# Kernel optimization log

Measured on AMD Instinct MI355X. Metric: run time of the kernel, lower is better.

The kernel has to match this reference:

```python
import jax, jax.numpy as jnp
import numpy as np

B, SQ, SK, D = 8, 2048, 2048, 128


def setup_inputs() -> dict:
    key = jax.random.key(0)
    kq, kk, kv = jax.random.split(key, 3)
    Q = jax.random.normal(kq, (B, SQ, D), dtype=jnp.float32)
    K = jax.random.normal(kk, (B, SK, D), dtype=jnp.float32)
    V = jax.random.normal(kv, (B, SK, D), dtype=jnp.float32)
    return {"Q": Q, "K": K, "V": V}


def reference(Q, K, V):
    d_k = K.shape[2]  # NOTE: module divides by d_k, not sqrt(d_k)
    # scores: [B, Sq, Sk]
    scores = jnp.einsum('bqd,bkd->bqk', Q, K) / d_k
    # unconventional softmax over the batch dim (dim=0), as in the source
    attn = jax.nn.softmax(scores, axis=0)
    # output: [B, Sq, D]
    return jnp.einsum('bqk,bkd->bqd', attn, V)
```

## Files before the change

kernel.cpp:

```cpp
#include <hip/hip_runtime.h>
#include <hip/hip_bf16.h>

#define B_   8
#define SQ_  2048
#define SK_  2048
#define D_   128

typedef __attribute__((ext_vector_type(8))) _Float16 f16x8;
typedef __attribute__((ext_vector_type(4))) _Float16 f16x4;
typedef __attribute__((ext_vector_type(4))) float    f32x4;

#define QK_BSTRIDE (128 * 4 * 64 * 8)
#define VF_BSTRIDE (64 * 8 * 64 * 8)

__device__ __forceinline__ void dma16(const void* g, void* l) {
    __builtin_amdgcn_global_load_lds(
        (const __attribute__((address_space(1))) unsigned int*)g,
        (__attribute__((address_space(3))) unsigned int*)l, 16, 0, 0);
}

__device__ __forceinline__ float fast_exp2(float x) {
#if __has_builtin(__builtin_amdgcn_exp2f)
    return __builtin_amdgcn_exp2f(x);
#else
    return __expf(x * 0.6931471805599453f);
#endif
}

__global__ __launch_bounds__(256)
void prep(const float* __restrict__ Q, const float* __restrict__ K,
          const float* __restrict__ V,
          _Float16* __restrict__ Qf, _Float16* __restrict__ Kf,
          _Float16* __restrict__ Vf) {
    __shared__ _Float16 T[64][136];
    const int bid = blockIdx.x;
    const int t   = threadIdx.x;
    if (bid < 512) {
        const int tens = bid >> 8;
        const float* src = tens ? K : Q;
        _Float16*    dst = tens ? Kf : Qf;
        const float  sc  = tens ? 0.0625f : 0.18033688f;
        const int b  = (bid >> 5) & 7;
        const int rb = bid & 31;
        const int row = t >> 2, c0 = (t & 3) * 32;
        const float* srow = src + ((size_t)b * 2048 + rb * 64 + row) * 128 + c0;
#pragma unroll
        for (int u = 0; u < 32; u += 4) {
            f32x4 v = *(const f32x4*)(srow + u);
            f16x4 h;
            h[0] = (_Float16)(v[0] * sc); h[1] = (_Float16)(v[1] * sc);
            h[2] = (_Float16)(v[2] * sc); h[3] = (_Float16)(v[3] * sc);
            *(f16x4*)&T[row][c0 + u] = h;
        }
        __syncthreads();
#pragma unroll
        for (int u = 0; u < 4; ++u) {
            int c  = u * 256 + t;
            int l  = c & 63;
            int ks = (c >> 6) & 3;
            int qt = c >> 8;
            int hi = l >> 4, ql = l & 15;
            f16x8 r = *(const f16x8*)&T[qt * 16 + ql][ks * 32 + hi * 8];
            *(f16x8*)(dst + ((((size_t)b * 128 + rb * 4 + qt) * 4 + ks) * 64 + l) * 8) = r;
        }
    } else {
        const int vb = bid - 512;
        const int b  = vb >> 5;
        const int kb = vb & 31;
        const int row = t >> 2, c0 = (t & 3) * 32;
        const float* src = V + ((size_t)b * SK_ + kb * 64 + row) * D_ + c0;
#pragma unroll
        for (int u = 0; u < 8; ++u) {
            f32x4 v = *(const f32x4*)(src + u * 4);
            f16x4 h;
            h[0] = (_Float16)v[0]; h[1] = (_Float16)v[1];
            h[2] = (_Float16)v[2]; h[3] = (_Float16)v[3];
            *(f16x4*)&T[row][c0 + u * 4] = h;
        }
        __syncthreads();
#pragma unroll
        for (int u = 0; u < 4; ++u) {
            int s   = u * 256 + t;
            int l   = s & 63;
            int dt  = (s >> 6) & 7;
            int ktl = s >> 9;
            int hi  = l >> 4, ql = l & 15;
            f16x8 r;
#pragma unroll
            for (int j = 0; j < 8; ++j) r[j] = T[ktl * 32 + hi * 8 + j][dt * 16 + ql];
            *(f16x8*)(Vf + (((size_t)b * 64 + kb * 2 + ktl) * 8 + dt) * 512 + (size_t)l * 8) = r;
        }
    }
}

__global__ __launch_bounds__(512, 4)
void zred(const _Float16* __restrict__ Qf, const _Float16* __restrict__ Kf,
          _Float16* __restrict__ Pf, int nqt, int qoff16) {
    __shared__ __attribute__((aligned(16))) _Float16 E[8][64][64];
    const int bid   = blockIdx.x;
    const int qtile = bid >> 5;
    const int ktile = bid & 31;
    const int b  = threadIdx.x >> 6;
    const int l  = threadIdx.x & 63;
    const int hi = l >> 4, ql = l & 15;

    const _Float16* Qb = Qf + (size_t)b * QK_BSTRIDE;
    const _Float16* Kb = Kf + (size_t)b * QK_BSTRIDE;

    f32x4 s[4][4] = {};
    __builtin_amdgcn_s_setprio(1);
#pragma unroll
    for (int ks = 0; ks < 4; ++ks) {
        f16x8 kf[4];
#pragma unroll
        for (int kk = 0; kk < 4; ++kk)
            kf[kk] = *(const f16x8*)(Kb + ((((size_t)ktile * 4 + kk) * 4 + ks) * 64 + l) * 8);
#pragma unroll
        for (int qq = 0; qq < 4; ++qq) {
            f16x8 qv = *(const f16x8*)(Qb + ((((size_t)(qoff16 + qtile * 4 + qq)) * 4 + ks) * 64 + l) * 8);
#pragma unroll
            for (int kk = 0; kk < 4; ++kk)
                s[kk][qq] = __builtin_amdgcn_mfma_f32_16x16x32_f16(kf[kk], qv, s[kk][qq], 0, 0, 0);
        }
    }
    __builtin_amdgcn_s_setprio(0);

    f16x4* E4 = (f16x4*)&E[0][0][0];
#pragma unroll
    for (int kk = 0; kk < 4; ++kk)
#pragma unroll
        for (int qq = 0; qq < 4; ++qq) {
            f16x4 e;
#pragma unroll
            for (int r = 0; r < 4; ++r)
                e[r] = (_Float16)fast_exp2(s[kk][qq][r]);
            int q = qq * 16 + ql;
            int k = kk * 16 + hi * 4;
            int g16 = ((b * 64 + q) << 3) + ((k >> 3) ^ (q & 7));
            E4[g16 * 2 + ((k >> 2) & 1)] = e;
        }
    __syncthreads();

    const int t    = threadIdx.x;
    const int ktl  = t >> 8;
    const int qq2  = (t >> 6) & 3;
    const int l2   = t & 63;
    const int hi2  = l2 >> 4, ql2 = l2 & 15;
    const int q_loc  = qq2 * 16 + ql2;
    const int k0_loc = ktl * 32 + hi2 * 8;
    const f16x8* E8  = (const f16x8*)&E[0][0][0];
    const int eidx   = (q_loc << 3) + ((k0_loc >> 3) ^ (q_loc & 7));

    f16x8 z = E8[eidx];
#pragma unroll
    for (int bb = 1; bb < 8; ++bb) z = z + E8[bb * 512 + eidx];
    float inv[8];
#pragma unroll
    for (int j = 0; j < 8; ++j) inv[j] = __builtin_amdgcn_rcpf((float)z[j]);

    const size_t pbase = (((size_t)(qtile * 4 + qq2)) * 64 + (ktile * 2 + ktl)) * 512 + (size_t)l2 * 8;
#pragma unroll
    for (int bb = 0; bb < 8; ++bb) {
        f16x8 e = E8[bb * 512 + eidx];
        f16x8 p;
#pragma unroll
        for (int j = 0; j < 8; ++j) p[j] = (_Float16)((float)e[j] * inv[j]);
        *(f16x8*)(Pf + (size_t)bb * nqt * 32768 + pbase) = p;
    }
}

__global__ __launch_bounds__(512)
void av(const _Float16* __restrict__ Pf, const _Float16* __restrict__ Vf,
        float* __restrict__ out, int nqt, int qoff) {
    __shared__ __attribute__((aligned(16))) _Float16 lds[4 * 12288];

    const int bid = blockIdx.x;
    const int b   = bid & 7;
    const int mt  = bid >> 3;
    const int w   = threadIdx.x >> 6;
    const int l   = threadIdx.x & 63;
    const int wq  = w >> 2;
    const int wd  = w & 3;
    const int hi  = l >> 4, ql = l & 15;

    const _Float16* Pb = Pf + (size_t)b * nqt * 32768;
    const _Float16* Vb = Vf + (size_t)b * VF_BSTRIDE;

#define STAGE(bufi, kt2) do {                                                  \
    _Float16* dst0 = (_Float16*)lds + (size_t)(bufi) * 12288;                  \
    _Pragma("unroll")                                                          \
    for (int u = 0; u < 3; ++u) {                                              \
        int c = w * 3 + u;                                                     \
        const _Float16* srcp;                                                  \
        if (c < 8)                                                             \
            srcp = Pb + (((size_t)(mt * 4 + (c >> 1))) * 64 + ((kt2) * 2 + (c & 1))) * 512 + (size_t)l * 8; \
        else {                                                                 \
            int cv = c - 8;                                                    \
            srcp = Vb + (((size_t)((kt2) * 2 + (cv >> 3))) * 8 + (cv & 7)) * 512 + (size_t)l * 8; \
        }                                                                      \
        dma16(srcp, dst0 + c * 512);                                           \
    }                                                                          \
} while (0)

#define MFMA_PHASE(bufi) do {                                                  \
    const _Float16* Bf = (const _Float16*)lds + (size_t)(bufi) * 12288;        \
    _Pragma("unroll")                                                          \
    for (int ktl = 0; ktl < 2; ++ktl) {                                        \
        f16x8 pfr[2], vfr[2];                                                  \
        _Pragma("unroll")                                                      \
        for (int i = 0; i < 2; ++i)                                            \
            pfr[i] = *(const f16x8*)(Bf + ((wq * 2 + i) * 2 + ktl) * 512 + l * 8); \
        _Pragma("unroll")                                                      \
        for (int j = 0; j < 2; ++j)                                            \
            vfr[j] = *(const f16x8*)(Bf + 4096 + (ktl * 8 + wd * 2 + j) * 512 + l * 8); \
        _Pragma("unroll")                                                      \
        for (int i = 0; i < 2; ++i)                                            \
            _Pragma("unroll")                                                  \
            for (int j = 0; j < 2; ++j)                                        \
                acc[i][j] = __builtin_amdgcn_mfma_f32_16x16x32_f16(pfr[i], vfr[j], acc[i][j], 0, 0, 0); \
    }                                                                          \
} while (0)

    f32x4 acc[2][2] = {};
    STAGE(0, 0);
    STAGE(1, 1);
    STAGE(2, 2);
    for (int kt2 = 0; kt2 < 32; ++kt2) {
        if (kt2 <= 29)      asm volatile("s_waitcnt vmcnt(6)" ::: "memory");
        else if (kt2 == 30) asm volatile("s_waitcnt vmcnt(3)" ::: "memory");
        else                asm volatile("s_waitcnt vmcnt(0)" ::: "memory");
        __builtin_amdgcn_s_barrier();
        __builtin_amdgcn_sched_barrier(0);
        if (kt2 < 29) STAGE((kt2 + 3) & 3, kt2 + 3);
        __builtin_amdgcn_s_setprio(1);
        MFMA_PHASE(kt2 & 3);
        __builtin_amdgcn_s_setprio(0);
    }

    const int q0 = qoff + mt * 64 + wq * 32;
#pragma unroll
    for (int i = 0; i < 2; ++i)
#pragma unroll
        for (int j = 0; j < 2; ++j)
#pragma unroll
            for (int r = 0; r < 4; ++r)
                out[((size_t)b * SQ_ + q0 + i * 16 + hi * 4 + r) * D_ + (wd * 2 + j) * 16 + ql]
                    = acc[i][j][r];
#undef STAGE
#undef MFMA_PHASE
}

extern "C" void kernel_launch(void* const* d_in, const int* in_sizes, int n_in,
                              void* d_out, int out_size, void* d_ws, size_t ws_size,
                              hipStream_t stream) {
    const float* Q = (const float*)d_in[0];
    const float* K = (const float*)d_in[1];
    const float* V = (const float*)d_in[2];
    float* out = (float*)d_out;

    _Float16* Qf = (_Float16*)d_ws;
    _Float16* Kf = Qf + (size_t)B_ * QK_BSTRIDE;
    _Float16* Vf = Kf + (size_t)B_ * QK_BSTRIDE;
    _Float16* Pf = Vf + (size_t)B_ * VF_BSTRIDE;

    size_t used  = (size_t)(12 * 1024 * 1024);
    size_t avail = ws_size > used ? (ws_size - used) / 2 : 0;
    int nq = 2048;
    while (nq > 64 && (size_t)nq * 16384 > avail) nq >>= 1;
    int nchunks = 2048 / nq;
    int nqt = nq / 16;

    prep<<<768, 256, 0, stream>>>(Q, K, V, Qf, Kf, Vf);

    for (int ci = 0; ci < nchunks; ++ci) {
        int qoff = ci * nq;
        zred<<<(nq / 64) * 32, 512, 0, stream>>>(Qf, Kf, Pf, nqt, qoff >> 4);
        av<<<(nq / 64) * 8, 512, 0, stream>>>(Pf, Vf, out, nqt, qoff);
    }
}
```

Measured before the change: 57.45 us.

## Fuse prep, score-softmax and AV kernels into one persistent kernel with grid barriers

Three separate launches (prep, zred, av) become a single persistent 256-block kernel. Phases are separated by a software grid barrier built from an atomic counter and spin-wait, and each block loops over several work items per phase. The chunking loop that sized the query range to the workspace is dropped, so the full P buffer must now fit, and a memset for the barrier is added. The goal is to remove launch gaps and tail effects, at the cost of a smaller grid (fewer blocks in flight in the zred phase), spin-barrier overhead, and a deadlock risk if not all 256 blocks are co-resident.

```diff
diff --git a/kernel.cpp b/kernel.cpp
--- a/kernel.cpp
+++ b/kernel.cpp
@@ -5,6 +5,7 @@
 #define SQ_  2048
 #define SK_  2048
 #define D_   128
+#define GRID 256
 
 typedef __attribute__((ext_vector_type(8))) _Float16 f16x8;
 typedef __attribute__((ext_vector_type(4))) _Float16 f16x4;
@@ -12,6 +13,7 @@
 
 #define QK_BSTRIDE (128 * 4 * 64 * 8)
 #define VF_BSTRIDE (64 * 8 * 64 * 8)
+#define P_BSTRIDE  ((size_t)128 * 64 * 512)
 
 __device__ __forceinline__ void dma16(const void* g, void* l) {
     __builtin_amdgcn_global_load_lds(
@@ -27,167 +29,191 @@
 #endif
 }
 
-__global__ __launch_bounds__(256)
-void prep(const float* __restrict__ Q, const float* __restrict__ K,
+__device__ __forceinline__ void gbar(unsigned* bar) {
+    __syncthreads();
+    if (threadIdx.x == 0) {
+        unsigned* ctr = bar;
+        unsigned* gen = bar + 32;
+        unsigned g = __hip_atomic_load(gen, __ATOMIC_RELAXED, __HIP_MEMORY_SCOPE_AGENT);
+        unsigned a = __hip_atomic_fetch_add(ctr, 1u, __ATOMIC_ACQ_REL, __HIP_MEMORY_SCOPE_AGENT);
+        if (a == GRID - 1) {
+            __hip_atomic_store(ctr, 0u, __ATOMIC_RELAXED, __HIP_MEMORY_SCOPE_AGENT);
+            __hip_atomic_store(gen, g + 1u, __ATOMIC_RELEASE, __HIP_MEMORY_SCOPE_AGENT);
+        } else {
+            long long t0 = clock64();
+            while (__hip_atomic_load(gen, __ATOMIC_ACQUIRE, __HIP_MEMORY_SCOPE_AGENT) == g) {
+                __builtin_amdgcn_s_sleep(32);
+                if (clock64() - t0 > 2000000000LL) break;
+            }
+        }
+    }
+    __syncthreads();
+}
+
+__global__ __launch_bounds__(512)
+void mega(const float* __restrict__ Q, const float* __restrict__ K,
           const float* __restrict__ V,
           _Float16* __restrict__ Qf, _Float16* __restrict__ Kf,
-          _Float16* __restrict__ Vf) {
-    __shared__ _Float16 T[64][136];
+          _Float16* __restrict__ Vf, _Float16* __restrict__ Pf,
+          unsigned* __restrict__ bar, float* __restrict__ out) {
+    __shared__ __attribute__((aligned(16))) char smem[98304];
+
     const int bid = blockIdx.x;
     const int t   = threadIdx.x;
-    if (bid < 512) {
-        const int tens = bid >> 8;
-        const float* src = tens ? K : Q;
-        _Float16*    dst = tens ? Kf : Qf;
-        const float  sc  = tens ? 0.0625f : 0.18033688f;
-        const int b  = (bid >> 5) & 7;
-        const int rb = bid & 31;
-        const int row = t >> 2, c0 = (t & 3) * 32;
-        const float* srow = src + ((size_t)b * 2048 + rb * 64 + row) * 128 + c0;
-#pragma unroll
-        for (int u = 0; u < 32; u += 4) {
-            f32x4 v = *(const f32x4*)(srow + u);
-            f16x4 h;
-            h[0] = (_Float16)(v[0] * sc); h[1] = (_Float16)(v[1] * sc);
-            h[2] = (_Float16)(v[2] * sc); h[3] = (_Float16)(v[3] * sc);
-            *(f16x4*)&T[row][c0 + u] = h;
-        }
-        __syncthreads();
-#pragma unroll
-        for (int u = 0; u < 4; ++u) {
-            int c  = u * 256 + t;
-            int l  = c & 63;
-            int ks = (c >> 6) & 3;
-            int qt = c >> 8;
-            int hi = l >> 4, ql = l & 15;
-            f16x8 r = *(const f16x8*)&T[qt * 16 + ql][ks * 32 + hi * 8];
-            *(f16x8*)(dst + ((((size_t)b * 128 + rb * 4 + qt) * 4 + ks) * 64 + l) * 8) = r;
-        }
-    } else {
-        const int vb = bid - 512;
-        const int b  = vb >> 5;
-        const int kb = vb & 31;
-        const int row = t >> 2, c0 = (t & 3) * 32;
-        const float* src = V + ((size_t)b * SK_ + kb * 64 + row) * D_ + c0;
-#pragma unroll
-        for (int u = 0; u < 8; ++u) {
-            f32x4 v = *(const f32x4*)(src + u * 4);
-            f16x4 h;
-            h[0] = (_Float16)v[0]; h[1] = (_Float16)v[1];
-            h[2] = (_Float16)v[2]; h[3] = (_Float16)v[3];
-            *(f16x4*)&T[row][c0 + u * 4] = h;
-        }
-        __syncthreads();
-#pragma unroll
-        for (int u = 0; u < 4; ++u) {
-            int s   = u * 256 + t;
-            int l   = s & 63;
-            int dt  = (s >> 6) & 7;
-            int ktl = s >> 9;
-            int hi  = l >> 4, ql = l & 15;
-            f16x8 r;
-#pragma unroll
-            for (int j = 0; j < 8; ++j) r[j] = T[ktl * 32 + hi * 8 + j][dt * 16 + ql];
-            *(f16x8*)(Vf + (((size_t)b * 64 + kb * 2 + ktl) * 8 + dt) * 512 + (size_t)l * 8) = r;
-        }
-    }
-}
-
-__global__ __launch_bounds__(512, 4)
-void zred(const _Float16* __restrict__ Qf, const _Float16* __restrict__ Kf,
-          _Float16* __restrict__ Pf, int nqt, int qoff16) {
-    __shared__ __attribute__((aligned(16))) _Float16 E[8][64][64];
-    const int bid   = blockIdx.x;
-    const int qtile = bid >> 5;
-    const int ktile = bid & 31;
-    const int b  = threadIdx.x >> 6;
-    const int l  = threadIdx.x & 63;
-    const int hi = l >> 4, ql = l & 15;
-
-    const _Float16* Qb = Qf + (size_t)b * QK_BSTRIDE;
-    const _Float16* Kb = Kf + (size_t)b * QK_BSTRIDE;
-
-    f32x4 s[4][4] = {};
-    __builtin_amdgcn_s_setprio(1);
-#pragma unroll
-    for (int ks = 0; ks < 4; ++ks) {
-        f16x8 kf[4];
-#pragma unroll
-        for (int kk = 0; kk < 4; ++kk)
-            kf[kk] = *(const f16x8*)(Kb + ((((size_t)ktile * 4 + kk) * 4 + ks) * 64 + l) * 8);
-#pragma unroll
-        for (int qq = 0; qq < 4; ++qq) {
-            f16x8 qv = *(const f16x8*)(Qb + ((((size_t)(qoff16 + qtile * 4 + qq)) * 4 + ks) * 64 + l) * 8);
+    const int w   = t >> 6;
+    const int l   = t & 63;
+    const int hi  = l >> 4, ql = l & 15;
+
+    {
+        _Float16 (*T)[136] = (_Float16 (*)[136])smem;
+#pragma unroll 1
+        for (int u = bid; u < 512; u += GRID) {
+            if (u < 256) {
+                const int   tens = u >> 7;
+                const float* src = tens ? K : Q;
+                _Float16*    dst = tens ? Kf : Qf;
+                const float  sc  = tens ? 0.0625f : 0.18033688f;
+                const int b  = (u >> 4) & 7;
+                const int rb = u & 15;
+                const int row = t >> 2, c0 = (t & 3) * 32;
+                const float* srow = src + ((size_t)b * SQ_ + rb * 128 + row) * D_ + c0;
+#pragma unroll
+                for (int j = 0; j < 32; j += 4) {
+                    f32x4 v = *(const f32x4*)(srow + j);
+                    f16x4 h;
+                    h[0] = (_Float16)(v[0] * sc); h[1] = (_Float16)(v[1] * sc);
+                    h[2] = (_Float16)(v[2] * sc); h[3] = (_Float16)(v[3] * sc);
+                    *(f16x4*)&T[row][c0 + j] = h;
+                }
+                __syncthreads();
+#pragma unroll
+                for (int it = 0; it < 4; ++it) {
+                    int c  = it * 512 + t;
+                    int ll = c & 63;
+                    int ks = (c >> 6) & 3;
+                    int qt = c >> 8;
+                    f16x8 r = *(const f16x8*)&T[qt * 16 + (ll & 15)][ks * 32 + (ll >> 4) * 8];
+                    *(f16x8*)(dst + ((((size_t)b * 128 + rb * 8 + qt) * 4 + ks) * 64 + ll) * 8) = r;
+                }
+            } else {
+                const int vu = u - 256;
+                const int b  = vu >> 5;
+                const int kb = vu & 31;
+                const int row = t >> 3, c0 = (t & 7) * 16;
+                const float* srow = V + ((size_t)b * SK_ + kb * 64 + row) * D_ + c0;
+#pragma unroll
+                for (int j = 0; j < 16; j += 4) {
+                    f32x4 v = *(const f32x4*)(srow + j);
+                    f16x4 h;
+                    h[0] = (_Float16)v[0]; h[1] = (_Float16)v[1];
+                    h[2] = (_Float16)v[2]; h[3] = (_Float16)v[3];
+                    *(f16x4*)&T[row][c0 + j] = h;
+                }
+                __syncthreads();
+#pragma unroll
+                for (int it = 0; it < 2; ++it) {
+                    int s   = it * 512 + t;
+                    int ll  = s & 63;
+                    int dt  = (s >> 6) & 7;
+                    int ktl = s >> 9;
+                    int lhi = ll >> 4, lql = ll & 15;
+                    f16x8 r;
+#pragma unroll
+                    for (int j = 0; j < 8; ++j) r[j] = T[ktl * 32 + lhi * 8 + j][dt * 16 + lql];
+                    *(f16x8*)(Vf + (((size_t)b * 64 + kb * 2 + ktl) * 8 + dt) * 512 + (size_t)ll * 8) = r;
+                }
+            }
+            __syncthreads();
+        }
+    }
+    gbar(bar);
+
+    {
+        _Float16* E  = (_Float16*)smem;
+        f16x4*    E4 = (f16x4*)smem;
+        const f16x8* E8 = (const f16x8*)smem;
+        const _Float16* Qb = Qf + (size_t)w * QK_BSTRIDE;
+        const _Float16* Kb = Kf + (size_t)w * QK_BSTRIDE;
+#pragma unroll 1
+        for (int i = 0; i < 4; ++i) {
+            const int z     = bid * 4 + i;
+            const int qtile = z >> 5;
+            const int ktile = z & 31;
+
+            f32x4 s[4][4] = {};
+            __builtin_amdgcn_s_setprio(1);
+#pragma unroll
+            for (int ks = 0; ks < 4; ++ks) {
+                f16x8 kf[4];
+#pragma unroll
+                for (int kk = 0; kk < 4; ++kk)
+                    kf[kk] = *(const f16x8*)(Kb + ((((size_t)ktile * 4 + kk) * 4 + ks) * 64 + l) * 8);
+#pragma unroll
+                for (int qq = 0; qq < 4; ++qq) {
+                    f16x8 qv = *(const f16x8*)(Qb + ((((size_t)qtile * 4 + qq) * 4 + ks) * 64 + l) * 8);
+#pragma unroll
+                    for (int kk = 0; kk < 4; ++kk)
+                        s[kk][qq] = __builtin_amdgcn_mfma_f32_16x16x32_f16(kf[kk], qv, s[kk][qq], 0, 0, 0);
+                }
+            }
+            __builtin_amdgcn_s_setprio(0);
+
 #pragma unroll
             for (int kk = 0; kk < 4; ++kk)
-                s[kk][qq] = __builtin_amdgcn_mfma_f32_16x16x32_f16(kf[kk], qv, s[kk][qq], 0, 0, 0);
-        }
-    }
-    __builtin_amdgcn_s_setprio(0);
-
-    f16x4* E4 = (f16x4*)&E[0][0][0];
-#pragma unroll
-    for (int kk = 0; kk < 4; ++kk)
-#pragma unroll
-        for (int qq = 0; qq < 4; ++qq) {
-            f16x4 e;
-#pragma unroll
-            for (int r = 0; r < 4; ++r)
-                e[r] = (_Float16)fast_exp2(s[kk][qq][r]);
-            int q = qq * 16 + ql;
-            int k = kk * 16 + hi * 4;
-            int g16 = ((b * 64 + q) << 3) + ((k >> 3) ^ (q & 7));
-            E4[g16 * 2 + ((k >> 2) & 1)] = e;
-        }
-    __syncthreads();
-
-    const int t    = threadIdx.x;
-    const int ktl  = t >> 8;
-    const int qq2  = (t >> 6) & 3;
-    const int l2   = t & 63;
-    const int hi2  = l2 >> 4, ql2 = l2 & 15;
-    const int q_loc  = qq2 * 16 + ql2;
-    const int k0_loc = ktl * 32 + hi2 * 8;
-    const f16x8* E8  = (const f16x8*)&E[0][0][0];
-    const int eidx   = (q_loc << 3) + ((k0_loc >> 3) ^ (q_loc & 7));
-
-    f16x8 z = E8[eidx];
-#pragma unroll
-    for (int bb = 1; bb < 8; ++bb) z = z + E8[bb * 512 + eidx];
-    float inv[8];
-#pragma unroll
-    for (int j = 0; j < 8; ++j) inv[j] = __builtin_amdgcn_rcpf((float)z[j]);
-
-    const size_t pbase = (((size_t)(qtile * 4 + qq2)) * 64 + (ktile * 2 + ktl)) * 512 + (size_t)l2 * 8;
-#pragma unroll
-    for (int bb = 0; bb < 8; ++bb) {
-        f16x8 e = E8[bb * 512 + eidx];
-        f16x8 p;
-#pragma unroll
-        for (int j = 0; j < 8; ++j) p[j] = (_Float16)((float)e[j] * inv[j]);
-        *(f16x8*)(Pf + (size_t)bb * nqt * 32768 + pbase) = p;
-    }
-}
-
-__global__ __launch_bounds__(512)
-void av(const _Float16* __restrict__ Pf, const _Float16* __restrict__ Vf,
-        float* __restrict__ out, int nqt, int qoff) {
-    __shared__ __attribute__((aligned(16))) _Float16 lds[4 * 12288];
-
-    const int bid = blockIdx.x;
-    const int b   = bid & 7;
-    const int mt  = bid >> 3;
-    const int w   = threadIdx.x >> 6;
-    const int l   = threadIdx.x & 63;
-    const int wq  = w >> 2;
-    const int wd  = w & 3;
-    const int hi  = l >> 4, ql = l & 15;
-
-    const _Float16* Pb = Pf + (size_t)b * nqt * 32768;
-    const _Float16* Vb = Vf + (size_t)b * VF_BSTRIDE;
+#pragma unroll
+                for (int qq = 0; qq < 4; ++qq) {
+                    f16x4 e;
+#pragma unroll
+                    for (int r = 0; r < 4; ++r)
+                        e[r] = (_Float16)fast_exp2(s[kk][qq][r]);
+                    int q = qq * 16 + ql;
+                    int k = kk * 16 + hi * 4;
+                    int g16 = ((w * 64 + q) << 3) + ((k >> 3) ^ (q & 7));
+                    E4[g16 * 2 + ((k >> 2) & 1)] = e;
+                }
+            __syncthreads();
+
+            const int ktl  = t >> 8;
+            const int qq2  = (t >> 6) & 3;
+            const int l2   = t & 63;
+            const int q_loc  = qq2 * 16 + (l2 & 15);
+            const int k0_loc = ktl * 32 + (l2 >> 4) * 8;
+            const int eidx   = (q_loc << 3) + ((k0_loc >> 3) ^ (q_loc & 7));
+
+            f16x8 zsum = E8[eidx];
+#pragma unroll
+            for (int bb = 1; bb < 8; ++bb) zsum = zsum + E8[bb * 512 + eidx];
+            float inv[8];
+#pragma unroll
+            for (int j = 0; j < 8; ++j) inv[j] = __builtin_amdgcn_rcpf((float)zsum[j]);
+
+            const size_t pbase = (((size_t)(qtile * 4 + qq2)) * 64 + (ktile * 2 + ktl)) * 512
+                               + (size_t)l2 * 8;
+#pragma unroll
+            for (int bb = 0; bb < 8; ++bb) {
+                f16x8 e = E8[bb * 512 + eidx];
+                f16x8 p;
+#pragma unroll
+                for (int j = 0; j < 8; ++j) p[j] = (_Float16)((float)e[j] * inv[j]);
+                *(f16x8*)(Pf + (size_t)bb * P_BSTRIDE + pbase) = p;
+            }
+            __syncthreads();
+        }
+    }
+    gbar(bar);
+
+    {
+        _Float16* lds = (_Float16*)smem;
+        const int b  = bid & 7;
+        const int mt = bid >> 3;
+        const int wq = w >> 2;
+        const int wd = w & 3;
+
+        const _Float16* Pb = Pf + (size_t)b * P_BSTRIDE;
+        const _Float16* Vb = Vf + (size_t)b * VF_BSTRIDE;
 
 #define STAGE(bufi, kt2) do {                                                  \
-    _Float16* dst0 = (_Float16*)lds + (size_t)(bufi) * 12288;                  \
+    _Float16* dst0 = lds + (size_t)(bufi) * 12288;                             \
     _Pragma("unroll")                                                          \
     for (int u = 0; u < 3; ++u) {                                              \
         int c = w * 3 + u;                                                     \
@@ -203,7 +229,7 @@
 } while (0)
 
 #define MFMA_PHASE(bufi) do {                                                  \
-    const _Float16* Bf = (const _Float16*)lds + (size_t)(bufi) * 12288;        \
+    const _Float16* Bf = lds + (size_t)(bufi) * 12288;                         \
     _Pragma("unroll")                                                          \
     for (int ktl = 0; ktl < 2; ++ktl) {                                        \
         f16x8 pfr[2], vfr[2];                                                  \
@@ -221,33 +247,34 @@
     }                                                                          \
 } while (0)
 
-    f32x4 acc[2][2] = {};
-    STAGE(0, 0);
-    STAGE(1, 1);
-    STAGE(2, 2);
-    for (int kt2 = 0; kt2 < 32; ++kt2) {
-        if (kt2 <= 29)      asm volatile("s_waitcnt vmcnt(6)" ::: "memory");
-        else if (kt2 == 30) asm volatile("s_waitcnt vmcnt(3)" ::: "memory");
-        else                asm volatile("s_waitcnt vmcnt(0)" ::: "memory");
-        __builtin_amdgcn_s_barrier();
-        __builtin_amdgcn_sched_barrier(0);
-        if (kt2 < 29) STAGE((kt2 + 3) & 3, kt2 + 3);
-        __builtin_amdgcn_s_setprio(1);
-        MFMA_PHASE(kt2 & 3);
-        __builtin_amdgcn_s_setprio(0);
-    }
-
-    const int q0 = qoff + mt * 64 + wq * 32;
-#pragma unroll
-    for (int i = 0; i < 2; ++i)
-#pragma unroll
-        for (int j = 0; j < 2; ++j)
-#pragma unroll
-            for (int r = 0; r < 4; ++r)
-                out[((size_t)b * SQ_ + q0 + i * 16 + hi * 4 + r) * D_ + (wd * 2 + j) * 16 + ql]
-                    = acc[i][j][r];
+        f32x4 acc[2][2] = {};
+        STAGE(0, 0);
+        STAGE(1, 1);
+        STAGE(2, 2);
+        for (int kt2 = 0; kt2 < 32; ++kt2) {
+            if (kt2 <= 29)      asm volatile("s_waitcnt vmcnt(6)" ::: "memory");
+            else if (kt2 == 30) asm volatile("s_waitcnt vmcnt(3)" ::: "memory");
+            else                asm volatile("s_waitcnt vmcnt(0)" ::: "memory");
+            __builtin_amdgcn_s_barrier();
+            __builtin_amdgcn_sched_barrier(0);
+            if (kt2 < 29) STAGE((kt2 + 3) & 3, kt2 + 3);
+            __builtin_amdgcn_s_setprio(1);
+            MFMA_PHASE(kt2 & 3);
+            __builtin_amdgcn_s_setprio(0);
+        }
+
+        const int q0 = mt * 64 + wq * 32;
+#pragma unroll
+        for (int i = 0; i < 2; ++i)
+#pragma unroll
+            for (int j = 0; j < 2; ++j)
+#pragma unroll
+                for (int r = 0; r < 4; ++r)
+                    out[((size_t)b * SQ_ + q0 + i * 16 + hi * 4 + r) * D_ + (wd * 2 + j) * 16 + ql]
+                        = acc[i][j][r];
 #undef STAGE
 #undef MFMA_PHASE
+    }
 }
 
 extern "C" void kernel_launch(void* const* d_in, const int* in_sizes, int n_in,
@@ -260,21 +287,11 @@
 
     _Float16* Qf = (_Float16*)d_ws;
     _Float16* Kf = Qf + (size_t)B_ * QK_BSTRIDE;
-    _Float16* Vf = Kf + (size_t)B_ * QK_BSTRIDE;
+    _Float16* Kend = Kf + (size_t)B_ * QK_BSTRIDE;
+    _Float16* Vf = Kend;
     _Float16* Pf = Vf + (size_t)B_ * VF_BSTRIDE;
-
-    size_t used  = (size_t)(12 * 1024 * 1024);
-    size_t avail = ws_size > used ? (ws_size - used) / 2 : 0;
-    int nq = 2048;
-    while (nq > 64 && (size_t)nq * 16384 > avail) nq >>= 1;
-    int nchunks = 2048 / nq;
-    int nqt = nq / 16;
-
-    prep<<<768, 256, 0, stream>>>(Q, K, V, Qf, Kf, Vf);
-
-    for (int ci = 0; ci < nchunks; ++ci) {
-        int qoff = ci * nq;
-        zred<<<(nq / 64) * 32, 512, 0, stream>>>(Qf, Kf, Pf, nqt, qoff >> 4);
-        av<<<(nq / 64) * 8, 512, 0, stream>>>(Pf, Vf, out, nqt, qoff);
-    }
-}
+    unsigned* bar = (unsigned*)((char*)d_ws + (size_t)128 * 1024 * 1024);
+
+    hipMemsetAsync(bar, 0, 256, stream);
+    mega<<<GRID, 512, 0, stream>>>(Q, K, V, Qf, Kf, Vf, Pf, bar, out);
+}
```

Measured after the change: 108.8 us, median of 2. 1.89x slower.
